# Performance work log

Hardware: AMD Instinct MI355X
Metric: run time of the kernel (lower is better)

Reference implementation:

```python
import jax, jax.numpy as jnp
import numpy as np

B, N, W, R, C, CIN, LOUT = 64, 1024, 64, 4, 512, 256, 256
IFACE = R * W + R + W + 1 + 2 * W + R + 2 + 3 * R  # 471
LIN = C + R * W


def setup_inputs() -> dict:
    key = jax.random.key(0)
    ks = jax.random.split(key, 18)
    s = 0.05
    return {
        "x": jax.random.normal(ks[0], (B, CIN), jnp.float32),
        "read": jax.random.uniform(ks[1], (B, R * W), jnp.float32) * 0.1,
        "h": jax.random.normal(ks[2], (B, C), jnp.float32) * 0.1,
        "c": jax.random.normal(ks[3], (B, C), jnp.float32) * 0.1,
        "memory": jax.random.normal(ks[4], (B, N, W), jnp.float32) * 0.1,
        "link": jax.random.uniform(ks[5], (B, N, N), jnp.float32) * 1e-3,
        "r_weights": jax.random.uniform(ks[6], (B, R, N), jnp.float32) / N,
        "w_weights": jax.random.uniform(ks[7], (B, N), jnp.float32) / N,
        "usage": jax.random.uniform(ks[8], (B, N), jnp.float32),
        "precedence": jax.random.uniform(ks[9], (B, N), jnp.float32) / N,
        "W_ih": jax.random.normal(ks[10], (4 * C, CIN + R * W), jnp.float32) * s,
        "W_hh": jax.random.normal(ks[11], (4 * C, C), jnp.float32) * s,
        "b_ih": jnp.zeros((4 * C,), jnp.float32),
        "b_hh": jnp.zeros((4 * C,), jnp.float32),
        "W_if": jax.random.normal(ks[12], (IFACE, C), jnp.float32) * s,
        "b_if": jnp.zeros((IFACE,), jnp.float32),
        "W_out": jax.random.normal(ks[13], (LOUT, LIN), jnp.float32) * s,
        "b_out": jnp.zeros((LOUT,), jnp.float32),
    }


def _dnc_step(x, read, h, c, memory, link, r_weights, w_weights, usage,
              precedence, W_ih, W_hh, b_ih, b_hh, W_if, b_if, W_out, b_out):
    Bb, Nn, Wd = memory.shape
    Rr = r_weights.shape[1]
    # --- LSTMCell controller (torch gate order i, f, g, o) ---
    inp = jnp.concatenate([x, read], axis=1)
    gates = inp @ W_ih.T + b_ih + h @ W_hh.T + b_hh
    i_g, f_g, g_g, o_g = jnp.split(gates, 4, axis=1)
    c_new = jax.nn.sigmoid(f_g) * c + jax.nn.sigmoid(i_g) * jnp.tanh(g_g)
    ctrl = jax.nn.sigmoid(o_g) * jnp.tanh(c_new)
    # --- interface vector split ---
    iface = ctrl @ W_if.T + b_if
    o = Rr * Wd
    r_keys = iface[:, :o].reshape(Bb, Rr, Wd)
    r_betas = iface[:, o:o + Rr]; o += Rr
    w_key = iface[:, o:o + Wd]; o += Wd
    w_beta = iface[:, o:o + 1]; o += 1
    e_vec = iface[:, o:o + Wd]; o += Wd
    w_vec = iface[:, o:o + Wd]; o += Wd
    f_gates = iface[:, o:o + Rr]; o += Rr
    a_gate = iface[:, o:o + 1]; o += 1
    w_gate = iface[:, o:o + 1]; o += 1
    r_modes = iface[:, o:o + 3 * Rr].reshape(Bb, Rr, 3)
    # --- allocation via sort + cumprod + scatter ---
    retention = jnp.prod(1.0 - jax.nn.sigmoid(f_gates)[:, :, None] * r_weights, axis=1)  # [B,N]
    usage_u = (usage + w_weights - usage * w_weights) * retention
    inds = jnp.argsort(usage_u, axis=1)
    sorted_u = jnp.take_along_axis(usage_u, inds, axis=1)
    before = (1.0 - sorted_u) * jnp.cumprod(sorted_u, axis=1)
    alloc = jnp.zeros_like(usage_u).at[jnp.arange(Bb)[:, None], inds].set(before)
    # --- write head: content addressing ---
    m_n = memory / (jnp.linalg.norm(memory, axis=2, keepdims=True) + 1e-8)
    wk = w_key / (jnp.linalg.norm(w_key, axis=1, keepdims=True) + 1e-8)
    w_c = jax.nn.softmax(jnp.einsum('bnw,bw->bn', m_n, wk) * (1.0 + jax.nn.softplus(w_beta)), axis=1)
    wg = jax.nn.sigmoid(w_gate)
    ag = jax.nn.sigmoid(a_gate)
    ev = jax.nn.sigmoid(e_vec)
    ww = wg * (ag * alloc + (1.0 - ag) * w_c)  # [B,N]
    # link matrix update (zero diagonal)
    link_new = (1.0 - ww[:, :, None] - ww[:, None, :]) * link + ww[:, :, None] * precedence[:, None, :]
    link_new = link_new * (1.0 - jnp.eye(Nn, dtype=link.dtype))
    # rank-1 erase + write
    mem_new = memory * (1.0 - ww[:, :, None] * ev[:, None, :]) + ww[:, :, None] * w_vec[:, None, :]
    prec_new = (1.0 - ww.sum(1, keepdims=True)) * precedence + ww
    # --- read heads (vectorized over R) ---
    mn2 = mem_new / (jnp.linalg.norm(mem_new, axis=2, keepdims=True) + 1e-8)
    rk = r_keys / (jnp.linalg.norm(r_keys, axis=2, keepdims=True) + 1e-8)
    r_c = jax.nn.softmax(jnp.einsum('bnw,brw->brn', mn2, rk) * (1.0 + jax.nn.softplus(r_betas))[:, :, None], axis=2)
    fwd = jnp.einsum('bnm,brm->brn', link_new, r_weights)   # forward weights
    bwd = jnp.einsum('bmn,brm->brn', link_new, r_weights)   # backward weights
    mode = jax.nn.softmax(r_modes, axis=2)
    rw_new = mode[:, :, 0:1] * bwd + mode[:, :, 1:2] * r_c + mode[:, :, 2:3] * fwd
    reads = jnp.einsum('brn,bnw->brw', rw_new, mem_new).reshape(Bb, Rr * Wd)
    out = jnp.concatenate([ctrl, reads], axis=1) @ W_out.T + b_out
    return out, reads, mem_new, link_new, rw_new, ww, usage_u, prec_new, ctrl, c_new


def reference(x, read, h, c, memory, link, r_weights, w_weights, usage,
              precedence, W_ih, W_hh, b_ih, b_hh, W_if, b_if, W_out, b_out):
    return _dnc_step(x, read, h, c, memory, link, r_weights, w_weights, usage,
                     precedence, W_ih, W_hh, b_ih, b_hh, W_if, b_if, W_out, b_out)
```

## Files before the change

kernel.cpp:

```cpp
#include <hip/hip_runtime.h>
#include <cmath>

#define Bb   64
#define Nn   1024
#define Wd   64
#define Rr   4
#define Cc   512
#define CINc 256
#define IFC  471

#define O_OUT    0
#define O_READS  16384
#define O_MEM    32768
#define O_LINK   4227072
#define O_RW     71335936
#define O_WW     71598080
#define O_USAGE  71663616
#define O_PREC   71729152
#define O_CTRL   71794688
#define O_CNEW   71827456

#define W_GATES  0
#define W_IFACE  131072
#define W_DER    161280
#define W_ALLOC  194048
#define W_SCW    259584
#define W_SCR    325120
#define W_FWD    587264
#define W_BWD    849408

__device__ __forceinline__ float sigf_(float x){ return 1.0f/(1.0f+expf(-x)); }
__device__ __forceinline__ float softplusf_(float x){ return fmaxf(x,0.0f) + log1pf(expf(-fabsf(x))); }
__device__ __forceinline__ float waveSum_(float v){
  #pragma unroll
  for (int o=32;o;o>>=1) v += __shfl_xor(v,o);
  return v;
}
__device__ __forceinline__ float waveMax_(float v){
  #pragma unroll
  for (int o=32;o;o>>=1) v = fmaxf(v, __shfl_xor(v,o));
  return v;
}

__global__ __launch_bounds__(256) void k_gates(
    const float* __restrict__ x, const float* __restrict__ rd,
    const float* __restrict__ h,
    const float* __restrict__ W_ih, const float* __restrict__ W_hh,
    const float* __restrict__ b_ih, const float* __restrict__ b_hh,
    float* __restrict__ gates)
{
  __shared__ __align__(16) float A1[512];
  __shared__ __align__(16) float A2[512];
  int b = blockIdx.y, t = threadIdx.x;
  for (int i=t;i<512;i+=256) A1[i] = (i<CINc)? x[b*CINc+i] : rd[b*256 + (i-CINc)];
  for (int i=t;i<512;i+=256) A2[i] = h[b*Cc+i];
  __syncthreads();
  int o = blockIdx.x*256 + t;
  const float4* w1 = reinterpret_cast<const float4*>(W_ih + (size_t)o*512);
  const float4* w2 = reinterpret_cast<const float4*>(W_hh + (size_t)o*Cc);
  const float4* a1 = reinterpret_cast<const float4*>(A1);
  const float4* a2 = reinterpret_cast<const float4*>(A2);
  float acc = b_ih[o] + b_hh[o];
  #pragma unroll 8
  for (int k=0;k<128;k++){ float4 w=w1[k], a=a1[k]; acc += w.x*a.x+w.y*a.y+w.z*a.z+w.w*a.w; }
  #pragma unroll 8
  for (int k=0;k<128;k++){ float4 w=w2[k], a=a2[k]; acc += w.x*a.x+w.y*a.y+w.z*a.z+w.w*a.w; }
  gates[(size_t)b*2048 + o] = acc;
}

__global__ __launch_bounds__(256) void k_lstm_pt(
    const float* __restrict__ gates, const float* __restrict__ c_old,
    float* __restrict__ c_new, float* __restrict__ ctrl)
{
  int idx = blockIdx.x*256 + threadIdx.x;
  int b = idx >> 9, j = idx & 511;
  const float* g = gates + (size_t)b*2048;
  float ig = sigf_(g[j]);
  float fg = sigf_(g[512+j]);
  float gg = tanhf(g[1024+j]);
  float og = sigf_(g[1536+j]);
  float cn = fg*c_old[idx] + ig*gg;
  c_new[idx] = cn;
  ctrl[idx]  = og*tanhf(cn);
}

__global__ __launch_bounds__(256) void k_iface(
    const float* __restrict__ ctrl, const float* __restrict__ W_if,
    const float* __restrict__ b_if, float* __restrict__ iface)
{
  __shared__ __align__(16) float A[512];
  int b = blockIdx.y, t = threadIdx.x;
  for (int i=t;i<512;i+=256) A[i]=ctrl[b*Cc+i];
  __syncthreads();
  int o = blockIdx.x*256+t;
  if (o >= IFC) return;
  const float4* w = reinterpret_cast<const float4*>(W_if + (size_t)o*Cc);
  const float4* a = reinterpret_cast<const float4*>(A);
  float acc = b_if[o];
  #pragma unroll 8
  for (int k=0;k<128;k++){ float4 wv=w[k], av=a[k]; acc += wv.x*av.x+wv.y*av.y+wv.z*av.z+wv.w*av.w; }
  iface[(size_t)b*IFC + o] = acc;
}

__global__ __launch_bounds__(64) void k_parse(
    const float* __restrict__ iface, float* __restrict__ der)
{
  int b = blockIdx.x, w = threadIdx.x;
  const float* f = iface + (size_t)b*IFC;
  float* D = der + (size_t)b*512;
  float wk = f[260+w];
  float wn = sqrtf(waveSum_(wk*wk)) + 1e-8f;
  D[32+w]  = wk/wn;
  D[96+w]  = sigf_(f[325+w]);
  D[160+w] = f[389+w];
  #pragma unroll
  for (int r=0;r<4;r++){
    float rk = f[r*64+w];
    float rn = sqrtf(waveSum_(rk*rk)) + 1e-8f;
    D[224 + r*64 + w] = rk/rn;
  }
  if (w < 4){
    D[w]   = sigf_(f[453+w]);
    D[4+w] = 1.0f + softplusf_(f[256+w]);
    float m0=f[459+w*3], m1=f[459+w*3+1], m2=f[459+w*3+2];
    float mx = fmaxf(m0,fmaxf(m1,m2));
    float e0=expf(m0-mx), e1=expf(m1-mx), e2=expf(m2-mx);
    float s = e0+e1+e2;
    D[12+w*3]   = e0/s;
    D[12+w*3+1] = e1/s;
    D[12+w*3+2] = e2/s;
  }
  if (w == 0){
    D[8]  = 1.0f + softplusf_(f[324]);
    D[9]  = sigf_(f[457]);
    D[10] = sigf_(f[458]);
  }
}

__global__ __launch_bounds__(256) void k_usage(
    const float* __restrict__ der, const float* __restrict__ r_w,
    const float* __restrict__ usage, const float* __restrict__ w_w,
    float* __restrict__ usage_u)
{
  int idx = blockIdx.x*256+threadIdx.x;
  int b = idx>>10, n = idx&1023;
  const float* D = der + (size_t)b*512;
  float ret = 1.0f;
  #pragma unroll
  for (int r=0;r<4;r++) ret *= (1.0f - D[r]*r_w[((size_t)b*4+r)*1024 + n]);
  float u = usage[idx], w = w_w[idx];
  usage_u[idx] = (u + w - u*w)*ret;
}

__global__ __launch_bounds__(1024) void k_sortalloc(
    const float* __restrict__ usage_u, float* __restrict__ alloc)
{
  __shared__ float sv[1024];
  __shared__ int   si[1024];
  __shared__ float sp[1024];
  int b = blockIdx.x, t = threadIdx.x;
  sv[t] = usage_u[b*1024+t];
  si[t] = t;
  __syncthreads();
  for (int k=2;k<=1024;k<<=1){
    for (int j=k>>1;j>0;j>>=1){
      int ixj = t ^ j;
      if (ixj > t){
        float a=sv[t], cc=sv[ixj];
        int ia=si[t], ic=si[ixj];
        bool up = ((t & k) == 0);
        bool gt = (a > cc) || (a==cc && ia > ic);
        if (up ? gt : !gt){ sv[t]=cc; sv[ixj]=a; si[t]=ic; si[ixj]=ia; }
      }
      __syncthreads();
    }
  }
  float myv = sv[t];
  sp[t] = myv;
  __syncthreads();
  for (int off=1; off<1024; off<<=1){
    float pl = (t>=off)? sp[t-off] : 1.0f;
    float pm = sp[t];
    __syncthreads();
    sp[t] = pm*pl;
    __syncthreads();
  }
  alloc[b*1024 + si[t]] = (1.0f - myv)*sp[t];
}

__global__ __launch_bounds__(256) void k_wscore(
    const float* __restrict__ mem, const float* __restrict__ der,
    float* __restrict__ scw)
{
  int t = threadIdx.x, lane = t&63;
  int row = blockIdx.x*4 + (t>>6);
  int b = row>>10;
  const float* D = der + (size_t)b*512;
  float m = mem[(size_t)row*64 + lane];
  float s1 = waveSum_(m * D[32+lane]);
  float s2 = waveSum_(m*m);
  if (lane==0) scw[row] = s1/(sqrtf(s2)+1e-8f) * D[8];
}

__global__ __launch_bounds__(256) void k_wwprec(
    const float* __restrict__ scw, const float* __restrict__ alloc,
    const float* __restrict__ der, const float* __restrict__ prec,
    float* __restrict__ ww, float* __restrict__ prec_new)
{
  __shared__ float sred[4];
  int b = blockIdx.x, t = threadIdx.x;
  int wave=t>>6, lane=t&63;
  const float* D = der + (size_t)b*512;
  float ag = D[9], wg = D[10];
  float s[4];
  #pragma unroll
  for (int k=0;k<4;k++) s[k] = scw[b*1024 + t + k*256];
  float mx = fmaxf(fmaxf(s[0],s[1]),fmaxf(s[2],s[3]));
  mx = waveMax_(mx);
  if (lane==0) sred[wave]=mx;
  __syncthreads();
  mx = fmaxf(fmaxf(sred[0],sred[1]),fmaxf(sred[2],sred[3]));
  __syncthreads();
  float e[4], lsum=0.0f;
  #pragma unroll
  for (int k=0;k<4;k++){ e[k]=expf(s[k]-mx); lsum+=e[k]; }
  lsum = waveSum_(lsum);
  if (lane==0) sred[wave]=lsum;
  __syncthreads();
  float S = sred[0]+sred[1]+sred[2]+sred[3];
  __syncthreads();
  float wv[4], wsum=0.0f;
  #pragma unroll
  for (int k=0;k<4;k++){
    int n = t + k*256;
    float wc = e[k]/S;
    wv[k] = wg*(ag*alloc[b*1024+n] + (1.0f-ag)*wc);
    ww[b*1024+n] = wv[k];
    wsum += wv[k];
  }
  wsum = waveSum_(wsum);
  if (lane==0) sred[wave]=wsum;
  __syncthreads();
  float T = sred[0]+sred[1]+sred[2]+sred[3];
  #pragma unroll
  for (int k=0;k<4;k++){
    int n = t + k*256;
    prec_new[b*1024+n] = (1.0f-T)*prec[b*1024+n] + wv[k];
  }
}

__global__ __launch_bounds__(256) void k_link(
    const float* __restrict__ link, const float* __restrict__ ww,
    const float* __restrict__ prec, const float* __restrict__ r_w,
    float* __restrict__ link_new, float* __restrict__ fwd, float* __restrict__ bwd)
{
  __shared__ __align__(16) float sP[1024];
  __shared__ __align__(16) float sW[1024];
  __shared__ __align__(16) float sR[4][1024];
  __shared__ float fpart[64][4][4];
  int b = blockIdx.y, g = blockIdx.x, t = threadIdx.x;
  int wave = t>>6, lane = t&63;
  for (int i=t;i<1024;i+=256){ sP[i]=prec[b*1024+i]; sW[i]=ww[b*1024+i]; }
  for (int i=t;i<4096;i+=256) sR[i>>10][i&1023] = r_w[(size_t)b*4096 + i];
  __syncthreads();
  int j0 = t*4;
  float4 wwj4 = *reinterpret_cast<const float4*>(&sW[j0]);
  float4 pj4  = *reinterpret_cast<const float4*>(&sP[j0]);
  float wwj[4] = {wwj4.x,wwj4.y,wwj4.z,wwj4.w};
  float pj[4]  = {pj4.x,pj4.y,pj4.z,pj4.w};
  float rj[4][4];
  #pragma unroll
  for (int r=0;r<4;r++){
    float4 v = *reinterpret_cast<const float4*>(&sR[r][j0]);
    rj[r][0]=v.x; rj[r][1]=v.y; rj[r][2]=v.z; rj[r][3]=v.w;
  }
  float bacc[4][4] = {{0.f}};
  const size_t base = ((size_t)b*1024 + g*64)*1024;
  for (int il=0; il<64; il++){
    int i = g*64 + il;
    float wwi = sW[i];
    float4 L4 = *reinterpret_cast<const float4*>(&link[base + (size_t)il*1024 + j0]);
    float Lq[4] = {L4.x, L4.y, L4.z, L4.w};
    float Ln[4];
    #pragma unroll
    for (int q=0;q<4;q++){
      float v = (1.0f - wwi - wwj[q])*Lq[q] + wwi*pj[q];
      Ln[q] = (i == j0+q) ? 0.0f : v;
    }
    float4 st; st.x=Ln[0]; st.y=Ln[1]; st.z=Ln[2]; st.w=Ln[3];
    *reinterpret_cast<float4*>(&link_new[base + (size_t)il*1024 + j0]) = st;
    float rwi0 = sR[0][i], rwi1 = sR[1][i], rwi2 = sR[2][i], rwi3 = sR[3][i];
    #pragma unroll
    for (int q=0;q<4;q++){
      bacc[0][q] += Ln[q]*rwi0;
      bacc[1][q] += Ln[q]*rwi1;
      bacc[2][q] += Ln[q]*rwi2;
      bacc[3][q] += Ln[q]*rwi3;
    }
    #pragma unroll
    for (int r=0;r<4;r++){
      float fa = Ln[0]*rj[r][0]+Ln[1]*rj[r][1]+Ln[2]*rj[r][2]+Ln[3]*rj[r][3];
      fa = waveSum_(fa);
      if (lane==0) fpart[il][r][wave]=fa;
    }
  }
  __syncthreads();
  {
    int row = t>>2, r = t&3;
    fwd[((size_t)b*4+r)*1024 + g*64 + row] =
      fpart[row][r][0]+fpart[row][r][1]+fpart[row][r][2]+fpart[row][r][3];
  }
  #pragma unroll
  for (int r=0;r<4;r++)
    #pragma unroll
    for (int q=0;q<4;q++)
      atomicAdd(&bwd[((size_t)b*4+r)*1024 + j0 + q], bacc[r][q]);
}

__global__ __launch_bounds__(256) void k_memnew(
    const float* __restrict__ mem, const float* __restrict__ ww,
    const float* __restrict__ der, float* __restrict__ mem_new,
    float* __restrict__ scr)
{
  int t = threadIdx.x, lane=t&63;
  int row = blockIdx.x*4 + (t>>6);
  int b = row>>10, n = row&1023;
  const float* D = der + (size_t)b*512;
  float wwn = ww[row];
  float m = mem[(size_t)row*64+lane];
  float v = m*(1.0f - wwn*D[96+lane]) + wwn*D[160+lane];
  mem_new[(size_t)row*64+lane] = v;
  float nrm = sqrtf(waveSum_(v*v)) + 1e-8f;
  float d0 = waveSum_(v*D[224+lane]);
  float d1 = waveSum_(v*D[224+64+lane]);
  float d2 = waveSum_(v*D[224+128+lane]);
  float d3 = waveSum_(v*D[224+192+lane]);
  if (lane==0){
    scr[((size_t)b*4+0)*1024+n] = d0/nrm*D[4];
    scr[((size_t)b*4+1)*1024+n] = d1/nrm*D[5];
    scr[((size_t)b*4+2)*1024+n] = d2/nrm*D[6];
    scr[((size_t)b*4+3)*1024+n] = d3/nrm*D[7];
  }
}

__global__ __launch_bounds__(256) void k_rc(
    const float* __restrict__ scr, const float* __restrict__ fwd,
    const float* __restrict__ bwd, const float* __restrict__ der,
    float* __restrict__ rw_new)
{
  __shared__ float sred[4];
  int br = blockIdx.x; int b = br>>2, r = br&3;
  int t = threadIdx.x, wave=t>>6, lane=t&63;
  const float* D = der + (size_t)b*512;
  float m0=D[12+r*3], m1=D[12+r*3+1], m2=D[12+r*3+2];
  float s[4];
  #pragma unroll
  for (int k=0;k<4;k++) s[k] = scr[(size_t)br*1024 + t + k*256];
  float mx = fmaxf(fmaxf(s[0],s[1]),fmaxf(s[2],s[3]));
  mx = waveMax_(mx);
  if (lane==0) sred[wave]=mx;
  __syncthreads();
  mx = fmaxf(fmaxf(sred[0],sred[1]),fmaxf(sred[2],sred[3]));
  __syncthreads();
  float e[4], lsum=0.0f;
  #pragma unroll
  for (int k=0;k<4;k++){ e[k]=expf(s[k]-mx); lsum+=e[k]; }
  lsum = waveSum_(lsum);
  if (lane==0) sred[wave]=lsum;
  __syncthreads();
  float S = sred[0]+sred[1]+sred[2]+sred[3];
  #pragma unroll
  for (int k=0;k<4;k++){
    size_t ix = (size_t)br*1024 + t + k*256;
    rw_new[ix] = m0*bwd[ix] + m1*(e[k]/S) + m2*fwd[ix];
  }
}

__global__ __launch_bounds__(256) void k_reads(
    const float* __restrict__ rw_new, const float* __restrict__ mem_new,
    float* __restrict__ reads)
{
  __shared__ float sRW[4][256];
  __shared__ float red[4][4][64];
  int chunk = blockIdx.x, b = blockIdx.y, t = threadIdx.x;
  int wave=t>>6, lane=t&63;
  for (int i=t;i<1024;i+=256)
    sRW[i>>8][i&255] = rw_new[(size_t)b*4096 + (size_t)(i>>8)*1024 + chunk*256 + (i&255)];
  __syncthreads();
  float acc0=0.f, acc1=0.f, acc2=0.f, acc3=0.f;
  int nbase = chunk*256 + wave*64;
  const float* mp = mem_new + ((size_t)b*1024 + nbase)*64 + lane;
  #pragma unroll 4
  for (int nn=0;nn<64;nn++){
    float v = mp[(size_t)nn*64];
    int nl = wave*64+nn;
    acc0 += sRW[0][nl]*v;
    acc1 += sRW[1][nl]*v;
    acc2 += sRW[2][nl]*v;
    acc3 += sRW[3][nl]*v;
  }
  red[wave][0][lane]=acc0; red[wave][1][lane]=acc1;
  red[wave][2][lane]=acc2; red[wave][3][lane]=acc3;
  __syncthreads();
  { int r=t>>6, l=t&63;
    float v = red[0][r][l]+red[1][r][l]+red[2][r][l]+red[3][r][l];
    atomicAdd(&reads[b*256 + r*64 + l], v); }
}

__global__ __launch_bounds__(256) void k_out(
    const float* __restrict__ ctrl, const float* __restrict__ reads,
    const float* __restrict__ W_out, const float* __restrict__ b_out,
    float* __restrict__ out)
{
  __shared__ __align__(16) float A[768];
  int b = blockIdx.x, t = threadIdx.x;
  for (int i=t;i<768;i+=256) A[i] = (i<512)? ctrl[b*512+i] : reads[b*256 + (i-512)];
  __syncthreads();
  const float4* w = reinterpret_cast<const float4*>(W_out + (size_t)t*768);
  const float4* a = reinterpret_cast<const float4*>(A);
  float acc = b_out[t];
  #pragma unroll 8
  for (int k=0;k<192;k++){ float4 wv=w[k], av=a[k]; acc += wv.x*av.x+wv.y*av.y+wv.z*av.z+wv.w*av.w; }
  out[b*256+t] = acc;
}

extern "C" void kernel_launch(void* const* d_in, const int* in_sizes, int n_in,
                              void* d_out, int out_size, void* d_ws, size_t ws_size,
                              hipStream_t stream)
{
  const float* x      = (const float*)d_in[0];
  const float* rd     = (const float*)d_in[1];
  const float* h      = (const float*)d_in[2];
  const float* c      = (const float*)d_in[3];
  const float* mem    = (const float*)d_in[4];
  const float* link   = (const float*)d_in[5];
  const float* r_w    = (const float*)d_in[6];
  const float* w_w    = (const float*)d_in[7];
  const float* usage  = (const float*)d_in[8];
  const float* prec   = (const float*)d_in[9];
  const float* W_ih   = (const float*)d_in[10];
  const float* W_hh   = (const float*)d_in[11];
  const float* b_ih   = (const float*)d_in[12];
  const float* b_hh   = (const float*)d_in[13];
  const float* W_if   = (const float*)d_in[14];
  const float* b_if   = (const float*)d_in[15];
  const float* W_out  = (const float*)d_in[16];
  const float* b_out  = (const float*)d_in[17];

  float* out = (float*)d_out;
  float* o_out   = out + O_OUT;
  float* o_reads = out + O_READS;
  float* o_mem   = out + O_MEM;
  float* o_link  = out + O_LINK;
  float* o_rw    = out + O_RW;
  float* o_ww    = out + O_WW;
  float* o_usage = out + O_USAGE;
  float* o_prec  = out + O_PREC;
  float* o_ctrl  = out + O_CTRL;
  float* o_cnew  = out + O_CNEW;

  float* ws = (float*)d_ws;
  float* w_gates = ws + W_GATES;
  float* w_iface = ws + W_IFACE;
  float* w_der   = ws + W_DER;
  float* w_alloc = ws + W_ALLOC;
  float* w_scw   = ws + W_SCW;
  float* w_scr   = ws + W_SCR;
  float* w_fwd   = ws + W_FWD;
  float* w_bwd   = ws + W_BWD;

  hipMemsetAsync(w_bwd,   0, 262144*sizeof(float), stream);
  hipMemsetAsync(o_reads, 0, 16384*sizeof(float),  stream);

  k_gates   <<<dim3(8,64),  256, 0, stream>>>(x, rd, h, W_ih, W_hh, b_ih, b_hh, w_gates);
  k_lstm_pt <<<128,         256, 0, stream>>>(w_gates, c, o_cnew, o_ctrl);
  k_iface   <<<dim3(2,64),  256, 0, stream>>>(o_ctrl, W_if, b_if, w_iface);
  k_parse   <<<64,           64, 0, stream>>>(w_iface, w_der);
  k_usage   <<<256,         256, 0, stream>>>(w_der, r_w, usage, w_w, o_usage);
  k_sortalloc<<<64,        1024, 0, stream>>>(o_usage, w_alloc);
  k_wscore  <<<16384,       256, 0, stream>>>(mem, w_der, w_scw);
  k_wwprec  <<<64,          256, 0, stream>>>(w_scw, w_alloc, w_der, prec, o_ww, o_prec);
  k_link    <<<dim3(16,64), 256, 0, stream>>>(link, o_ww, prec, r_w, o_link, w_fwd, w_bwd);
  k_memnew  <<<16384,       256, 0, stream>>>(mem, o_ww, w_der, o_mem, w_scr);
  k_rc      <<<256,         256, 0, stream>>>(w_scr, w_fwd, w_bwd, w_der, o_rw);
  k_reads   <<<dim3(4,64),  256, 0, stream>>>(o_rw, o_mem, o_reads);
  k_out     <<<64,          256, 0, stream>>>(o_ctrl, o_reads, W_out, b_out, o_out);
}
```

Baseline: 741.8 us.

## Split link kernel into smaller row tiles with register prefetch and slimmer LDS

```diff
diff --git a/kernel.cpp b/kernel.cpp
--- a/kernel.cpp
+++ b/kernel.cpp
@@ -254,42 +254,48 @@
     const float* __restrict__ prec, const float* __restrict__ r_w,
     float* __restrict__ link_new, float* __restrict__ fwd, float* __restrict__ bwd)
 {
-  __shared__ __align__(16) float sP[1024];
-  __shared__ __align__(16) float sW[1024];
-  __shared__ __align__(16) float sR[4][1024];
-  __shared__ float fpart[64][4][4];
+  __shared__ float sWrow[32];
+  __shared__ float sRrow[4][32];
+  __shared__ float fpart[32][4][4];
   int b = blockIdx.y, g = blockIdx.x, t = threadIdx.x;
   int wave = t>>6, lane = t&63;
-  for (int i=t;i<1024;i+=256){ sP[i]=prec[b*1024+i]; sW[i]=ww[b*1024+i]; }
-  for (int i=t;i<4096;i+=256) sR[i>>10][i&1023] = r_w[(size_t)b*4096 + i];
-  __syncthreads();
+
+  if (t < 32) sWrow[t] = ww[b*1024 + g*32 + t];
+  else if (t < 160){ int r=(t-32)>>5, i=(t-32)&31;
+    sRrow[r][i] = r_w[(size_t)b*4096 + (size_t)r*1024 + g*32 + i]; }
+
   int j0 = t*4;
-  float4 wwj4 = *reinterpret_cast<const float4*>(&sW[j0]);
-  float4 pj4  = *reinterpret_cast<const float4*>(&sP[j0]);
+  float4 wwj4 = *reinterpret_cast<const float4*>(ww   + b*1024 + j0);
+  float4 pj4  = *reinterpret_cast<const float4*>(prec + b*1024 + j0);
   float wwj[4] = {wwj4.x,wwj4.y,wwj4.z,wwj4.w};
   float pj[4]  = {pj4.x,pj4.y,pj4.z,pj4.w};
   float rj[4][4];
   #pragma unroll
   for (int r=0;r<4;r++){
-    float4 v = *reinterpret_cast<const float4*>(&sR[r][j0]);
+    float4 v = *reinterpret_cast<const float4*>(r_w + (size_t)b*4096 + (size_t)r*1024 + j0);
     rj[r][0]=v.x; rj[r][1]=v.y; rj[r][2]=v.z; rj[r][3]=v.w;
   }
+  __syncthreads();
+
+  const size_t base = ((size_t)b*1024 + (size_t)g*32)*1024;
+  const float* lp  = link     + base + j0;
+  float*       lnp = link_new + base + j0;
+
   float bacc[4][4] = {{0.f}};
-  const size_t base = ((size_t)b*1024 + g*64)*1024;
-  for (int il=0; il<64; il++){
-    int i = g*64 + il;
-    float wwi = sW[i];
-    float4 L4 = *reinterpret_cast<const float4*>(&link[base + (size_t)il*1024 + j0]);
-    float Lq[4] = {L4.x, L4.y, L4.z, L4.w};
+  float4 L = *reinterpret_cast<const float4*>(lp);
+  for (int il=0; il<32; il++){
+    float4 Lnext;
+    if (il < 31) Lnext = *reinterpret_cast<const float4*>(lp + (size_t)(il+1)*1024);
+    int i = g*32 + il;
+    float wwi = sWrow[il];
     float Ln[4];
-    #pragma unroll
-    for (int q=0;q<4;q++){
-      float v = (1.0f - wwi - wwj[q])*Lq[q] + wwi*pj[q];
-      Ln[q] = (i == j0+q) ? 0.0f : v;
-    }
+    Ln[0] = (i==j0  ) ? 0.0f : (1.0f-wwi-wwj[0])*L.x + wwi*pj[0];
+    Ln[1] = (i==j0+1) ? 0.0f : (1.0f-wwi-wwj[1])*L.y + wwi*pj[1];
+    Ln[2] = (i==j0+2) ? 0.0f : (1.0f-wwi-wwj[2])*L.z + wwi*pj[2];
+    Ln[3] = (i==j0+3) ? 0.0f : (1.0f-wwi-wwj[3])*L.w + wwi*pj[3];
     float4 st; st.x=Ln[0]; st.y=Ln[1]; st.z=Ln[2]; st.w=Ln[3];
-    *reinterpret_cast<float4*>(&link_new[base + (size_t)il*1024 + j0]) = st;
-    float rwi0 = sR[0][i], rwi1 = sR[1][i], rwi2 = sR[2][i], rwi3 = sR[3][i];
+    *reinterpret_cast<float4*>(lnp + (size_t)il*1024) = st;
+    float rwi0 = sRrow[0][il], rwi1 = sRrow[1][il], rwi2 = sRrow[2][il], rwi3 = sRrow[3][il];
     #pragma unroll
     for (int q=0;q<4;q++){
       bacc[0][q] += Ln[q]*rwi0;
@@ -303,11 +309,12 @@
       fa = waveSum_(fa);
       if (lane==0) fpart[il][r][wave]=fa;
     }
-  }
-  __syncthreads();
-  {
+    L = Lnext;
+  }
+  __syncthreads();
+  if (t < 128){
     int row = t>>2, r = t&3;
-    fwd[((size_t)b*4+r)*1024 + g*64 + row] =
+    fwd[((size_t)b*4+r)*1024 + g*32 + row] =
       fpart[row][r][0]+fpart[row][r][1]+fpart[row][r][2]+fpart[row][r][3];
   }
   #pragma unroll
@@ -480,7 +487,7 @@
   k_sortalloc<<<64,        1024, 0, stream>>>(o_usage, w_alloc);
   k_wscore  <<<16384,       256, 0, stream>>>(mem, w_der, w_scw);
   k_wwprec  <<<64,          256, 0, stream>>>(w_scw, w_alloc, w_der, prec, o_ww, o_prec);
-  k_link    <<<dim3(16,64), 256, 0, stream>>>(link, o_ww, prec, r_w, o_link, w_fwd, w_bwd);
+  k_link    <<<dim3(32,64), 256, 0, stream>>>(link, o_ww, prec, r_w, o_link, w_fwd, w_bwd);
   k_memnew  <<<16384,       256, 0, stream>>>(mem, o_ww, w_der, o_mem, w_scr);
   k_rc      <<<256,         256, 0, stream>>>(w_scr, w_fwd, w_bwd, w_der, o_rw);
   k_reads   <<<dim3(4,64),  256, 0, stream>>>(o_rw, o_mem, o_reads);
```

Measured after the change: 761.2 us. 2.6% more time.
